# Kernel optimization log

Measured on AMD Instinct MI355X. Metric: run time of the kernel, lower is better.

Reference implementation:

```python
import jax, jax.numpy as jnp
import numpy as np

ROUTINGS = 3
EPS = 1e-7  # K.epsilon()

B, IN_CAPS, IN_DIM = 32, 2048, 16
NUM_CAPS, DIM_CAPS = 32, 16


def setup_inputs() -> dict:
    key = jax.random.key(0)
    k1, k2 = jax.random.split(key)
    x = jax.random.normal(k1, (B, IN_CAPS, IN_DIM), dtype=jnp.float32)
    # glorot-uniform-ish scale for capsule weights
    limit = np.sqrt(6.0 / (IN_DIM + DIM_CAPS)).astype(np.float32)
    W = jax.random.uniform(k2, (1, IN_CAPS, NUM_CAPS, DIM_CAPS, IN_DIM),
                           dtype=jnp.float32, minval=-limit, maxval=limit)
    return {"x": x, "W": W}


def _squash(v, axis=-1):
    s = jnp.sum(v * v, axis=axis, keepdims=True)
    scale = s / (1.0 + s) / jnp.sqrt(s + EPS)
    return scale * v


def reference(x, W):
    # inputs_hat[b,i,n,d] = sum_k W[0,i,n,d,k] * x[b,i,k]
    u = jnp.einsum('indk,bik->bind', W[0], x)  # [B, in_caps, num_caps, dim_caps]
    b = jnp.zeros(u.shape[:3], dtype=u.dtype)  # routing logits [B, in_caps, num_caps]
    outputs = None
    for i in range(ROUTINGS):
        c = jax.nn.softmax(b, axis=2)               # over num_capsule
        weighted = u * c[..., None]                 # [B, in, num, dim]
        outputs = _squash(jnp.sum(weighted, axis=1))  # [B, num, dim]
        if i < ROUTINGS - 1:
            # faithful to source: b += sum_d inputs_hat * c (NOT agreement with outputs)
            b = b + jnp.sum(weighted, axis=-1)
    return outputs
```

## Files before the change

kernel.cpp:

```cpp
#include <hip/hip_runtime.h>
#include <cstdint>
#include <cstddef>

#define LOG2E 1.4426950408889634f

typedef float f4v __attribute__((ext_vector_type(4)));

template<int CTRL>
__device__ __forceinline__ float dpp_addf(float v) {
  const int s = __builtin_amdgcn_update_dpp(
      0, __builtin_bit_cast(int, v), CTRL, 0xF, 0xF, true);
  return v + __builtin_bit_cast(float, s);
}
#define DPP_XOR1     0xB1
#define DPP_XOR2     0x4E
#define DPP_HALF_MIR 0x141
#define DPP_ROW_MIR  0x140

__device__ __forceinline__ void gld_lds16(const float* g, float* l) {
  __builtin_amdgcn_global_load_lds(
      (const __attribute__((address_space(1))) void*)g,
      (__attribute__((address_space(3))) void*)l, 16, 0, 0);
}

__device__ __forceinline__ int swz(int b) { return b ^ ((b >> 3) & 7); }

__device__ __forceinline__ void stage_half(const float* Wg, float* buf,
                                           int wv, int ln) {
  #pragma unroll
  for (int t = 0; t < 2; ++t) {
    const int seg = ((wv << 1) + t) << 8;
    const int j   = swz((seg >> 2) + ln);
    gld_lds16(Wg + ((j >> 1) << 4) + ((j & 1) << 2), buf + seg);
  }
}

__device__ __forceinline__ void lds_barrier() {
  asm volatile("s_waitcnt lgkmcnt(0)\n\ts_barrier" ::: "memory");
}

__device__ __forceinline__ const float* uniform_fptr(const float* p) {
  const uint64_t u = (uint64_t)p;
  const uint32_t lo = __builtin_amdgcn_readfirstlane((uint32_t)u);
  const uint32_t hi = __builtin_amdgcn_readfirstlane((uint32_t)(u >> 32));
  return (const float*)(((uint64_t)hi << 32) | lo);
}

__device__ __forceinline__ void sload_x2(const float* p0, const float* p1,
                                         f4v& a0, f4v& a1, f4v& a2, f4v& a3,
                                         f4v& b0, f4v& b1, f4v& b2, f4v& b3) {
  asm volatile(
      "s_load_dwordx4 %0, %8, 0\n\t"
      "s_load_dwordx4 %1, %8, 16\n\t"
      "s_load_dwordx4 %2, %8, 32\n\t"
      "s_load_dwordx4 %3, %8, 48\n\t"
      "s_load_dwordx4 %4, %9, 0\n\t"
      "s_load_dwordx4 %5, %9, 16\n\t"
      "s_load_dwordx4 %6, %9, 32\n\t"
      "s_load_dwordx4 %7, %9, 48\n\t"
      "s_waitcnt lgkmcnt(0)"
      : "=&s"(a0), "=&s"(a1), "=&s"(a2), "=&s"(a3),
        "=&s"(b0), "=&s"(b1), "=&s"(b2), "=&s"(b3)
      : "s"(p0), "s"(p1));
}

template<bool ATOMIC>
__global__ __launch_bounds__(512)
void caps_main(const float* __restrict__ X, const float* __restrict__ Wt,
               float* __restrict__ part) {
  __shared__ float sW[2][4096];
  __shared__ float sWs[32 * 20];
  __shared__ float sC[32 * 36];
  __shared__ float sPad[3584];
  if ((int)blockIdx.x == -1) sPad[threadIdx.x] = 1.f;

  const int tid  = threadIdx.x;
  const int wv   = tid >> 6, ln = tid & 63;
  const int t256 = tid & 255;
  const int bh   = tid >> 8;
  const int i0   = blockIdx.x << 2;

  stage_half(Wt + ((size_t)i0 << 13), sW[0], wv, ln);

  const int bB = tid >> 4;
  const int n1 = tid & 15;
  const int j0 = t256 << 2;
  const int nr = t256 >> 3;

  float acc0[16], acc1[16];
  #pragma unroll
  for (int b = 0; b < 16; ++b) { acc0[b] = 0.f; acc1[b] = 0.f; }

  for (int ii = 0; ii < 4; ++ii) {
    const float* WtI = Wt + ((size_t)(i0 + ii) << 13);
    __syncthreads();

    const float* xg = X + ((size_t)bB << 15) + ((size_t)(i0 + ii) << 4);
    const float4 x0 = *(const float4*)(xg + 0);
    const float4 x1 = *(const float4*)(xg + 4);
    const float4 x2 = *(const float4*)(xg + 8);
    const float4 x3 = *(const float4*)(xg + 12);

    stage_half(WtI + 8, sW[1], wv, ln);

    const float4 wa0 = *(const float4*)&sW[0][swz(j0 + 0) << 2];
    const float4 wa1 = *(const float4*)&sW[0][swz(j0 + 1) << 2];
    const float4 wb0 = *(const float4*)&sW[0][swz(j0 + 2) << 2];
    const float4 wb1 = *(const float4*)&sW[0][swz(j0 + 3) << 2];

    __syncthreads();
    if (ii < 3) stage_half(WtI + 8192, sW[0], wv, ln);

    const float4 wa2 = *(const float4*)&sW[1][swz(j0 + 0) << 2];
    const float4 wa3 = *(const float4*)&sW[1][swz(j0 + 1) << 2];
    const float4 wb2 = *(const float4*)&sW[1][swz(j0 + 2) << 2];
    const float4 wb3 = *(const float4*)&sW[1][swz(j0 + 3) << 2];

    if (tid < 256) {
      float pr[16] = { wa0.x+wb0.x, wa0.y+wb0.y, wa0.z+wb0.z, wa0.w+wb0.w,
                       wa1.x+wb1.x, wa1.y+wb1.y, wa1.z+wb1.z, wa1.w+wb1.w,
                       wa2.x+wb2.x, wa2.y+wb2.y, wa2.z+wb2.z, wa2.w+wb2.w,
                       wa3.x+wb3.x, wa3.y+wb3.y, wa3.z+wb3.z, wa3.w+wb3.w };
      #pragma unroll
      for (int q = 0; q < 16; ++q) {
        float v = pr[q];
        v = dpp_addf<DPP_XOR1>(v);
        v = dpp_addf<DPP_XOR2>(v);
        v = dpp_addf<DPP_HALF_MIR>(v);
        pr[q] = v;
      }
      if ((tid & 7) < 4) {
        const int m = tid & 3;
        const float4 w =
            (m & 2) ? ((m & 1) ? make_float4(pr[12], pr[13], pr[14], pr[15])
                               : make_float4(pr[8],  pr[9],  pr[10], pr[11]))
                    : ((m & 1) ? make_float4(pr[4],  pr[5],  pr[6],  pr[7])
                               : make_float4(pr[0],  pr[1],  pr[2],  pr[3]));
        *(float4*)&sWs[(t256 >> 3) * 20 + (m << 2)] = w;
      }
    }
    lds_barrier();

    {
      float t1 = 0.f, t2 = 0.f;
      #pragma unroll
      for (int c4 = 0; c4 < 4; ++c4) {
        const float4 A1 = *(const float4*)&sWs[n1 * 20 + (c4 << 2)];
        const float4 A2 = *(const float4*)&sWs[(n1 + 16) * 20 + (c4 << 2)];
        const float4 xc = (c4 == 0) ? x0 : (c4 == 1) ? x1 : (c4 == 2) ? x2 : x3;
        t1 += A1.x * xc.x + A1.y * xc.y + A1.z * xc.z + A1.w * xc.w;
        t2 += A2.x * xc.x + A2.y * xc.y + A2.z * xc.z + A2.w * xc.w;
      }
      const float l1a = t1 * 0.03125f, l1b = t2 * 0.03125f;
      const float e1a = exp2f(l1a * LOG2E), e1b = exp2f(l1b * LOG2E);
      float s1 = e1a + e1b;
      s1 = dpp_addf<DPP_XOR1>(s1); s1 = dpp_addf<DPP_XOR2>(s1);
      s1 = dpp_addf<DPP_HALF_MIR>(s1); s1 = dpp_addf<DPP_ROW_MIR>(s1);
      const float rs1 = __builtin_amdgcn_rcpf(s1);
      const float l2a = l1a + e1a * rs1 * t1;
      const float l2b = l1b + e1b * rs1 * t2;
      const float e2a = exp2f(l2a * LOG2E), e2b = exp2f(l2b * LOG2E);
      float s2 = e2a + e2b;
      s2 = dpp_addf<DPP_XOR1>(s2); s2 = dpp_addf<DPP_XOR2>(s2);
      s2 = dpp_addf<DPP_HALF_MIR>(s2); s2 = dpp_addf<DPP_ROW_MIR>(s2);
      const float rs2 = __builtin_amdgcn_rcpf(s2);
      sC[n1 * 36 + bB]        = e2a * rs2;
      sC[(n1 + 16) * 36 + bB] = e2b * rs2;
    }
    lds_barrier();

    float c2s[16];
    {
      const int cb = nr * 36 + (bh << 4);
      *(float4*)&c2s[0]  = *(const float4*)&sC[cb + 0];
      *(float4*)&c2s[4]  = *(const float4*)&sC[cb + 4];
      *(float4*)&c2s[8]  = *(const float4*)&sC[cb + 8];
      *(float4*)&c2s[12] = *(const float4*)&sC[cb + 12];
    }
    const size_t xoff = ((size_t)(i0 + ii) << 4);
    const float* pbase = uniform_fptr(X + (((size_t)(bh << 4)) << 15) + xoff);
    #pragma unroll
    for (int cl = 0; cl < 8; ++cl) {
      const float* p0 = pbase + ((size_t)(cl << 1) << 15);
      const float* p1 = p0 + 32768;
      f4v xa0, xa1, xa2, xa3, xb0, xb1, xb2, xb3;
      sload_x2(p0, p1, xa0, xa1, xa2, xa3, xb0, xb1, xb2, xb3);
      float u0 = wa0.x*xa0.x + wa0.y*xa0.y + wa0.z*xa0.z + wa0.w*xa0.w
               + wa1.x*xa1.x + wa1.y*xa1.y + wa1.z*xa1.z + wa1.w*xa1.w
               + wa2.x*xa2.x + wa2.y*xa2.y + wa2.z*xa2.z + wa2.w*xa2.w
               + wa3.x*xa3.x + wa3.y*xa3.y + wa3.z*xa3.z + wa3.w*xa3.w;
      float u1 = wb0.x*xa0.x + wb0.y*xa0.y + wb0.z*xa0.z + wb0.w*xa0.w
               + wb1.x*xa1.x + wb1.y*xa1.y + wb1.z*xa1.z + wb1.w*xa1.w
               + wb2.x*xa2.x + wb2.y*xa2.y + wb2.z*xa2.z + wb2.w*xa2.w
               + wb3.x*xa3.x + wb3.y*xa3.y + wb3.z*xa3.z + wb3.w*xa3.w;
      float v0 = wa0.x*xb0.x + wa0.y*xb0.y + wa0.z*xb0.z + wa0.w*xb0.w
               + wa1.x*xb1.x + wa1.y*xb1.y + wa1.z*xb1.z + wa1.w*xb1.w
               + wa2.x*xb2.x + wa2.y*xb2.y + wa2.z*xb2.z + wa2.w*xb2.w
               + wa3.x*xb3.x + wa3.y*xb3.y + wa3.z*xb3.z + wa3.w*xb3.w;
      float v1 = wb0.x*xb0.x + wb0.y*xb0.y + wb0.z*xb0.z + wb0.w*xb0.w
               + wb1.x*xb1.x + wb1.y*xb1.y + wb1.z*xb1.z + wb1.w*xb1.w
               + wb2.x*xb2.x + wb2.y*xb2.y + wb2.z*xb2.z + wb2.w*xb2.w
               + wb3.x*xb3.x + wb3.y*xb3.y + wb3.z*xb3.z + wb3.w*xb3.w;
      acc0[(cl << 1)    ] += c2s[(cl << 1)    ] * u0;
      acc1[(cl << 1)    ] += c2s[(cl << 1)    ] * u1;
      acc0[(cl << 1) + 1] += c2s[(cl << 1) + 1] * v0;
      acc1[(cl << 1) + 1] += c2s[(cl << 1) + 1] * v1;
    }
  }

  if constexpr (ATOMIC) {
    #pragma unroll
    for (int j = 0; j < 16; ++j) {
      const int bgl = (bh << 4) + j;
      float* dst = part + ((size_t)bgl << 9) + (t256 << 1);
      atomicAdd(dst, acc0[j]);
      atomicAdd(dst + 1, acc1[j]);
    }
  } else {
    float* wp = part + ((size_t)blockIdx.x << 14) + (t256 << 1);
    #pragma unroll
    for (int j = 0; j < 16; ++j) {
      const int bgl = (bh << 4) + j;
      *(float2*)(wp + ((size_t)bgl << 9)) = make_float2(acc0[j], acc1[j]);
    }
  }
}

__global__ __launch_bounds__(512)
void caps_reduce(const float* __restrict__ part, float* __restrict__ out) {
  __shared__ float sred[32][64];
  const int tid = threadIdx.x;
  const int bid = blockIdx.x;
  const int b  = bid >> 3;
  const int rb = bid & 7;
  const int pg = tid >> 4;
  const int sl = tid & 15;
  const float* src = part + (((size_t)pg << 4) << 14)
                   + (b << 9) + (rb << 6) + (sl << 2);
  float4 a = make_float4(0.f, 0.f, 0.f, 0.f);
  #pragma unroll 4
  for (int p = 0; p < 16; ++p) {
    const float4 v = *(const float4*)(src + ((size_t)p << 14));
    a.x += v.x; a.y += v.y; a.z += v.z; a.w += v.w;
  }
  *(float4*)&sred[pg][sl << 2] = a;
  __syncthreads();
  if (tid < 64) {
    float s = 0.f;
    #pragma unroll
    for (int g = 0; g < 32; ++g) s += sred[g][tid];
    float sq = s * s;
    sq += __shfl_xor(sq, 1); sq += __shfl_xor(sq, 2);
    sq += __shfl_xor(sq, 4); sq += __shfl_xor(sq, 8);
    const float scale = sq / (1.0f + sq) / sqrtf(sq + 1e-7f);
    out[(b << 9) + (rb << 6) + tid] = scale * s;
  }
}

__global__ __launch_bounds__(256)
void caps_squash(const float* __restrict__ sums, float* __restrict__ out) {
  const int e = (blockIdx.x << 8) + threadIdx.x;
  const float s = sums[e];
  float sq = s * s;
  sq += __shfl_xor(sq, 1); sq += __shfl_xor(sq, 2);
  sq += __shfl_xor(sq, 4); sq += __shfl_xor(sq, 8);
  const float scale = sq / (1.0f + sq) / sqrtf(sq + 1e-7f);
  out[e] = scale * s;
}

extern "C" void kernel_launch(void* const* d_in, const int* in_sizes, int n_in,
                              void* d_out, int out_size, void* d_ws, size_t ws_size,
                              hipStream_t stream) {
  const float* X  = (const float*)d_in[0];
  const float* Wt = (const float*)d_in[1];
  float* out = (float*)d_out;
  float* wsf = (float*)d_ws;
  const size_t need = (size_t)512 * 16384 * sizeof(float);
  if (ws_size >= need) {
    caps_main<false><<<512, 512, 0, stream>>>(X, Wt, wsf);
    caps_reduce<<<256, 512, 0, stream>>>(wsf, out);
  } else {
    float* acc = (ws_size >= (size_t)16384 * sizeof(float)) ? wsf : out;
    hipMemsetAsync(acc, 0, 16384 * sizeof(float), stream);
    caps_main<true><<<512, 512, 0, stream>>>(X, Wt, acc);
    caps_squash<<<64, 256, 0, stream>>>(acc, out);
  }
}
```

Baseline: 48.56 us.

## Double-buffer full W tiles per input capsule and prefetch next x

Each LDS buffer now holds the whole W tile for one input capsule, and the two buffers alternate across iterations. The next tile is staged while the current one is consumed, so each iteration needs one barrier instead of two. The x loads for the next capsule are issued at the end of the current iteration, the loop is unrolled, and the launch bounds ask for two blocks per CU. Removing the LDS padding array and the change in LDS size alter occupancy. The barrier now waits on vmcnt(0), which can stall on the outstanding x prefetch as well as the W staging.

```diff
diff --git a/kernel.cpp b/kernel.cpp
--- a/kernel.cpp
+++ b/kernel.cpp
@@ -35,8 +35,17 @@
   }
 }
 
+__device__ __forceinline__ void stage_tile(const float* WtI, float* buf,
+                                           int wv, int ln) {
+  stage_half(WtI,     buf,        wv, ln);
+  stage_half(WtI + 8, buf + 4096, wv, ln);
+}
+
 __device__ __forceinline__ void lds_barrier() {
   asm volatile("s_waitcnt lgkmcnt(0)\n\ts_barrier" ::: "memory");
+}
+__device__ __forceinline__ void full_barrier() {
+  asm volatile("s_waitcnt vmcnt(0) lgkmcnt(0)\n\ts_barrier" ::: "memory");
 }
 
 __device__ __forceinline__ const float* uniform_fptr(const float* p) {
@@ -65,14 +74,12 @@
 }
 
 template<bool ATOMIC>
-__global__ __launch_bounds__(512)
+__global__ __launch_bounds__(512, 2)
 void caps_main(const float* __restrict__ X, const float* __restrict__ Wt,
                float* __restrict__ part) {
-  __shared__ float sW[2][4096];
+  __shared__ float sW[2][8192];
   __shared__ float sWs[32 * 20];
   __shared__ float sC[32 * 36];
-  __shared__ float sPad[3584];
-  if ((int)blockIdx.x == -1) sPad[threadIdx.x] = 1.f;
 
   const int tid  = threadIdx.x;
   const int wv   = tid >> 6, ln = tid & 63;
@@ -80,41 +87,40 @@
   const int bh   = tid >> 8;
   const int i0   = blockIdx.x << 2;
 
-  stage_half(Wt + ((size_t)i0 << 13), sW[0], wv, ln);
+  stage_tile(Wt + ((size_t)i0 << 13), sW[0], wv, ln);
 
   const int bB = tid >> 4;
   const int n1 = tid & 15;
   const int j0 = t256 << 2;
   const int nr = t256 >> 3;
 
+  const float* xg = X + ((size_t)bB << 15) + ((size_t)i0 << 4);
+  float4 x0 = *(const float4*)(xg + 0);
+  float4 x1 = *(const float4*)(xg + 4);
+  float4 x2 = *(const float4*)(xg + 8);
+  float4 x3 = *(const float4*)(xg + 12);
+
   float acc0[16], acc1[16];
   #pragma unroll
   for (int b = 0; b < 16; ++b) { acc0[b] = 0.f; acc1[b] = 0.f; }
 
+  #pragma unroll
   for (int ii = 0; ii < 4; ++ii) {
-    const float* WtI = Wt + ((size_t)(i0 + ii) << 13);
-    __syncthreads();
-
-    const float* xg = X + ((size_t)bB << 15) + ((size_t)(i0 + ii) << 4);
-    const float4 x0 = *(const float4*)(xg + 0);
-    const float4 x1 = *(const float4*)(xg + 4);
-    const float4 x2 = *(const float4*)(xg + 8);
-    const float4 x3 = *(const float4*)(xg + 12);
-
-    stage_half(WtI + 8, sW[1], wv, ln);
-
-    const float4 wa0 = *(const float4*)&sW[0][swz(j0 + 0) << 2];
-    const float4 wa1 = *(const float4*)&sW[0][swz(j0 + 1) << 2];
-    const float4 wb0 = *(const float4*)&sW[0][swz(j0 + 2) << 2];
-    const float4 wb1 = *(const float4*)&sW[0][swz(j0 + 3) << 2];
-
-    __syncthreads();
-    if (ii < 3) stage_half(WtI + 8192, sW[0], wv, ln);
-
-    const float4 wa2 = *(const float4*)&sW[1][swz(j0 + 0) << 2];
-    const float4 wa3 = *(const float4*)&sW[1][swz(j0 + 1) << 2];
-    const float4 wb2 = *(const float4*)&sW[1][swz(j0 + 2) << 2];
-    const float4 wb3 = *(const float4*)&sW[1][swz(j0 + 3) << 2];
+    const int p = ii & 1;
+    full_barrier();
+
+    if (ii < 3)
+      stage_tile(Wt + ((size_t)(i0 + ii + 1) << 13), sW[p ^ 1], wv, ln);
+
+    const float* sWp = &sW[p][0];
+    const float4 wa0 = *(const float4*)&sWp[swz(j0 + 0) << 2];
+    const float4 wa1 = *(const float4*)&sWp[swz(j0 + 1) << 2];
+    const float4 wb0 = *(const float4*)&sWp[swz(j0 + 2) << 2];
+    const float4 wb1 = *(const float4*)&sWp[swz(j0 + 3) << 2];
+    const float4 wa2 = *(const float4*)&sWp[4096 + (swz(j0 + 0) << 2)];
+    const float4 wa3 = *(const float4*)&sWp[4096 + (swz(j0 + 1) << 2)];
+    const float4 wb2 = *(const float4*)&sWp[4096 + (swz(j0 + 2) << 2)];
+    const float4 wb3 = *(const float4*)&sWp[4096 + (swz(j0 + 3) << 2)];
 
     if (tid < 256) {
       float pr[16] = { wa0.x+wb0.x, wa0.y+wb0.y, wa0.z+wb0.z, wa0.w+wb0.w,
@@ -206,6 +212,14 @@
       acc0[(cl << 1) + 1] += c2s[(cl << 1) + 1] * v0;
       acc1[(cl << 1) + 1] += c2s[(cl << 1) + 1] * v1;
     }
+
+    if (ii < 3) {
+      const float* xgn = X + ((size_t)bB << 15) + ((size_t)(i0 + ii + 1) << 4);
+      x0 = *(const float4*)(xgn + 0);
+      x1 = *(const float4*)(xgn + 4);
+      x2 = *(const float4*)(xgn + 8);
+      x3 = *(const float4*)(xgn + 12);
+    }
   }
 
   if constexpr (ATOMIC) {
```

New measurement: 99.52 us. +104.9%, slower.
